# Kernel optimization log

Hardware: AMD Instinct MI355X
Metric: run time of the kernel (lower is better)

Reference implementation:

```python
import jax, jax.numpy as jnp
import numpy as np

IN_FEATURES = 4096
OUT_FEATURES = 4096
TOKENS = 8192
DENSITY = 0.5


def setup_inputs() -> dict:
    key = jax.random.key(0)
    kx, kw, km, kb = jax.random.split(key, 4)
    X = jax.random.normal(kx, (TOKENS, IN_FEATURES), dtype=jnp.float32)
    # kaiming-uniform-like init for weight [out, in]
    bound_w = np.sqrt(6.0 / IN_FEATURES) / np.sqrt(1.0 + 5.0)
    W = jax.random.uniform(kw, (OUT_FEATURES, IN_FEATURES), dtype=jnp.float32,
                           minval=-bound_w, maxval=bound_w)
    mask = jax.random.bernoulli(km, DENSITY, (OUT_FEATURES, IN_FEATURES))
    bound_b = 1.0 / np.sqrt(IN_FEATURES)
    b = jax.random.uniform(kb, (OUT_FEATURES,), dtype=jnp.float32,
                           minval=-bound_b, maxval=bound_b)
    return {"X": X, "W": W, "mask": mask, "b": b}


def reference(X, W, mask, b):
    # F.linear with a fixed-mask sparse weight: y = X @ (W * mask)^T + b
    Wm = W * mask.astype(W.dtype)  # masked weight [out, in]
    return jnp.einsum('ti,oi->to', X, Wm) + b
```

## Files before the change

### kernel.cpp

```cpp
#include <hip/hip_runtime.h>
#include <hip/hip_bf16.h>
#include <cstdint>
#include <cstddef>

#define M_TOK 8192
#define K_IN  4096
#define N_OUT 4096

typedef __attribute__((ext_vector_type(8))) short short8;
typedef __attribute__((ext_vector_type(8))) unsigned short ushort8;
typedef __attribute__((ext_vector_type(4))) float f32x4;

__device__ inline void split_bf16(float x, unsigned short& h, unsigned short& l) {
    unsigned int u = __float_as_uint(x);
    unsigned int hb = (u + 0x7FFFu + ((u >> 16) & 1u)) >> 16;
    h = (unsigned short)hb;
    float hf = __uint_as_float(hb << 16);
    float r = x - hf;
    unsigned int ur = __float_as_uint(r);
    unsigned int lb = (ur + 0x7FFFu + ((ur >> 16) & 1u)) >> 16;
    l = (unsigned short)lb;
}

__global__ void sl_cvt_x(const float* __restrict__ X,
                         unsigned short* __restrict__ hi,
                         unsigned short* __restrict__ lo,
                         int ngroups) {
    int stride = gridDim.x * blockDim.x;
    for (int g = blockIdx.x * blockDim.x + threadIdx.x; g < ngroups; g += stride) {
        const float4* p = (const float4*)X + (size_t)g * 2;
        float4 a = p[0], b = p[1];
        float f[8] = {a.x, a.y, a.z, a.w, b.x, b.y, b.z, b.w};
        ushort8 h, l;
#pragma unroll
        for (int i = 0; i < 8; ++i) {
            unsigned short hh, ll;
            split_bf16(f[i], hh, ll);
            h[i] = hh; l[i] = ll;
        }
        *(ushort8*)(hi + (size_t)g * 8) = h;
        *(ushort8*)(lo + (size_t)g * 8) = l;
    }
}

__global__ void sl_cvt_w(const float* __restrict__ W,
                         const int* __restrict__ mask,
                         unsigned short* __restrict__ hi,
                         unsigned short* __restrict__ lo,
                         int ngroups) {
    int stride = gridDim.x * blockDim.x;
    for (int g = blockIdx.x * blockDim.x + threadIdx.x; g < ngroups; g += stride) {
        const float4* p = (const float4*)W + (size_t)g * 2;
        const int4*  mp = (const int4*)mask + (size_t)g * 2;
        float4 a = p[0], b = p[1];
        int4 ma = mp[0], mb = mp[1];
        float f[8];
        f[0] = ma.x ? a.x : 0.f;  f[1] = ma.y ? a.y : 0.f;
        f[2] = ma.z ? a.z : 0.f;  f[3] = ma.w ? a.w : 0.f;
        f[4] = mb.x ? b.x : 0.f;  f[5] = mb.y ? b.y : 0.f;
        f[6] = mb.z ? b.z : 0.f;  f[7] = mb.w ? b.w : 0.f;
        ushort8 h, l;
#pragma unroll
        for (int i = 0; i < 8; ++i) {
            unsigned short hh, ll;
            split_bf16(f[i], hh, ll);
            h[i] = hh; l[i] = ll;
        }
        *(ushort8*)(hi + (size_t)g * 8) = h;
        *(ushort8*)(lo + (size_t)g * 8) = l;
    }
}

__device__ inline void gload16(const void* g, void* l) {
    __builtin_amdgcn_global_load_lds(
        (const __attribute__((address_space(1))) void*)g,
        (__attribute__((address_space(3))) void*)l, 16, 0, 0);
}

__global__ __launch_bounds__(256, 3)
void sl_gemm_bf16x3(const unsigned short* __restrict__ Xhi,
                    const unsigned short* __restrict__ Xlo,
                    const unsigned short* __restrict__ Whi,
                    const unsigned short* __restrict__ Wlo,
                    const float* __restrict__ bias,
                    float* __restrict__ out) {
    __shared__ __align__(16) unsigned short At[128 * 64];
    __shared__ __align__(16) unsigned short Bt[128 * 64];

    const int bid = blockIdx.x;
    const int swz = (bid & 7) * 256 + (bid >> 3);
    const int bm = swz >> 5;
    const int bn = swz & 31;
    const int brow = bm * 128;
    const int bcol = bn * 128;

    const int tid = threadIdx.x;
    const int w   = tid >> 6;
    const int l   = tid & 63;
    const int wr  = w >> 1, wc = w & 1;

    const int rlo  = l >> 3;
    const int slot = l & 7;
    const int kb   = slot ^ rlo;
    const unsigned short* aBase = (kb < 4) ? Xhi : Xlo;
    const unsigned short* bBase = (kb < 4) ? Whi : Wlo;
    const int kboff = (kb & 3) * 8;

    const unsigned short* aSrc[4];
    const unsigned short* bSrc[4];
#pragma unroll
    for (int i = 0; i < 4; ++i) {
        const int ar = brow + w * 32 + i * 8 + rlo;
        const int br = bcol + w * 32 + i * 8 + rlo;
        aSrc[i] = aBase + (size_t)ar * K_IN + kboff;
        bSrc[i] = bBase + (size_t)br * K_IN + kboff;
    }

    const int lr = l & 15;
    const int kg = l >> 4;

    f32x4 acc[4][4];
#pragma unroll
    for (int i = 0; i < 4; ++i)
#pragma unroll
        for (int j = 0; j < 4; ++j)
            acc[i][j] = (f32x4){0.f, 0.f, 0.f, 0.f};

    for (int kt = 0; kt < K_IN / 32; ++kt) {
        const int koff = kt * 32;
#pragma unroll
        for (int i = 0; i < 4; ++i) {
            gload16(aSrc[i] + koff, (char*)At + (w * 4 + i) * 1024);
            gload16(bSrc[i] + koff, (char*)Bt + (w * 4 + i) * 1024);
        }
        __syncthreads();

        short8 bhi[4], blo[4];
#pragma unroll
        for (int j = 0; j < 4; ++j) {
            const int rowB = wc * 64 + j * 16 + lr;
            const int sw = rowB & 7;
            bhi[j] = *(const short8*)(Bt + rowB * 64 + ((kg ^ sw) << 3));
            blo[j] = *(const short8*)(Bt + rowB * 64 + (((kg + 4) ^ sw) << 3));
        }
#pragma unroll
        for (int i = 0; i < 4; ++i) {
            const int rowA = wr * 64 + i * 16 + lr;
            const int sw = rowA & 7;
            short8 ahi = *(const short8*)(At + rowA * 64 + ((kg ^ sw) << 3));
            short8 alo = *(const short8*)(At + rowA * 64 + (((kg + 4) ^ sw) << 3));
#pragma unroll
            for (int j = 0; j < 4; ++j) {
                acc[i][j] = __builtin_amdgcn_mfma_f32_16x16x32_bf16(ahi, bhi[j], acc[i][j], 0, 0, 0);
                acc[i][j] = __builtin_amdgcn_mfma_f32_16x16x32_bf16(ahi, blo[j], acc[i][j], 0, 0, 0);
                acc[i][j] = __builtin_amdgcn_mfma_f32_16x16x32_bf16(alo, bhi[j], acc[i][j], 0, 0, 0);
            }
        }
        __syncthreads();
    }

    float bv[4];
#pragma unroll
    for (int j = 0; j < 4; ++j)
        bv[j] = bias[bcol + wc * 64 + j * 16 + lr];
#pragma unroll
    for (int i = 0; i < 4; ++i) {
        const int trow = brow + wr * 64 + i * 16 + kg * 4;
#pragma unroll
        for (int j = 0; j < 4; ++j) {
            const int ocol = bcol + wc * 64 + j * 16 + lr;
#pragma unroll
            for (int r = 0; r < 4; ++r)
                out[(size_t)(trow + r) * N_OUT + ocol] = acc[i][j][r] + bv[j];
        }
    }
}

__global__ void sl_naive(const float* __restrict__ X, const float* __restrict__ W,
                         const int* __restrict__ mask, const float* __restrict__ bias,
                         float* __restrict__ out) {
    int o = blockIdx.x * blockDim.x + threadIdx.x;
    int t = blockIdx.y;
    if (o >= N_OUT) return;
    const float* xr = X + (size_t)t * K_IN;
    const float* wr = W + (size_t)o * K_IN;
    const int*   mr = mask + (size_t)o * K_IN;
    float s = 0.f;
    for (int k = 0; k < K_IN; ++k)
        s += xr[k] * (mr[k] ? wr[k] : 0.f);
    out[(size_t)t * N_OUT + o] = s + bias[o];
}

extern "C" void kernel_launch(void* const* d_in, const int* in_sizes, int n_in,
                              void* d_out, int out_size, void* d_ws, size_t ws_size,
                              hipStream_t stream) {
    (void)in_sizes; (void)n_in; (void)out_size;
    const float* X    = (const float*)d_in[0];
    const float* W    = (const float*)d_in[1];
    const int*   mask = (const int*)d_in[2];
    const float* bias = (const float*)d_in[3];
    float* out = (float*)d_out;

    const size_t xplane = (size_t)M_TOK * K_IN;
    const size_t wplane = (size_t)N_OUT * K_IN;
    const size_t need = (2 * xplane + 2 * wplane) * sizeof(unsigned short);

    if (ws_size < need) {
        dim3 g((N_OUT + 255) / 256, M_TOK);
        sl_naive<<<g, 256, 0, stream>>>(X, W, mask, bias, out);
        return;
    }

    unsigned short* Xhi = (unsigned short*)d_ws;
    unsigned short* Xlo = Xhi + xplane;
    unsigned short* Whi = Xlo + xplane;
    unsigned short* Wlo = Whi + wplane;

    sl_cvt_x<<<2048, 256, 0, stream>>>(X, Xhi, Xlo, (int)(xplane / 8));
    sl_cvt_w<<<2048, 256, 0, stream>>>(W, mask, Whi, Wlo, (int)(wplane / 8));
    sl_gemm_bf16x3<<<2048, 256, 0, stream>>>(Xhi, Xlo, Whi, Wlo, bias, out);
}
```

Measured before the change: 1.237 ms.

## Restructure bf16x3 GEMM into 256x256 tiles with a 4-stage async pipeline

Enlarges the GEMM block tile from 128x128 to 256x256 with 512 threads, and restructures the K loop so the three bf16 product passes (hi*hi, hi*lo, lo*hi) run as three sequential K segments of 128 steps each. It adds a 4-deep LDS ring buffer filled by direct global-to-LDS loads, with manual vmcnt waits, a single barrier per step, and MFMA priority hints. The aim is to hide memory latency and raise operand reuse per byte loaded. In exchange it uses more LDS and registers per block, giving lower occupancy and fewer blocks. The conversion kernels switch to 4-element vectors per thread.

Result: faster. 1.139 ms (-8.0%).

```diff
diff --git a/kernel.cpp b/kernel.cpp
--- a/kernel.cpp
+++ b/kernel.cpp
@@ -6,9 +6,10 @@
 #define M_TOK 8192
 #define K_IN  4096
 #define N_OUT 4096
+#define NKS   384
 
 typedef __attribute__((ext_vector_type(8))) short short8;
-typedef __attribute__((ext_vector_type(8))) unsigned short ushort8;
+typedef __attribute__((ext_vector_type(4))) unsigned short ushort4v;
 typedef __attribute__((ext_vector_type(4))) float f32x4;
 
 __device__ inline void split_bf16(float x, unsigned short& h, unsigned short& l) {
@@ -22,52 +23,45 @@
     l = (unsigned short)lb;
 }
 
-__global__ void sl_cvt_x(const float* __restrict__ X,
-                         unsigned short* __restrict__ hi,
-                         unsigned short* __restrict__ lo,
-                         int ngroups) {
+__global__ __launch_bounds__(256) void sl_cvt_x(const float* __restrict__ X,
+                                                unsigned short* __restrict__ hi,
+                                                unsigned short* __restrict__ lo, int n4) {
     int stride = gridDim.x * blockDim.x;
-    for (int g = blockIdx.x * blockDim.x + threadIdx.x; g < ngroups; g += stride) {
-        const float4* p = (const float4*)X + (size_t)g * 2;
-        float4 a = p[0], b = p[1];
-        float f[8] = {a.x, a.y, a.z, a.w, b.x, b.y, b.z, b.w};
-        ushort8 h, l;
-#pragma unroll
-        for (int i = 0; i < 8; ++i) {
+    for (int g = blockIdx.x * blockDim.x + threadIdx.x; g < n4; g += stride) {
+        float4 v = ((const float4*)X)[g];
+        float f[4] = {v.x, v.y, v.z, v.w};
+        ushort4v h, l;
+#pragma unroll
+        for (int i = 0; i < 4; ++i) {
             unsigned short hh, ll;
             split_bf16(f[i], hh, ll);
             h[i] = hh; l[i] = ll;
         }
-        *(ushort8*)(hi + (size_t)g * 8) = h;
-        *(ushort8*)(lo + (size_t)g * 8) = l;
-    }
-}
-
-__global__ void sl_cvt_w(const float* __restrict__ W,
-                         const int* __restrict__ mask,
-                         unsigned short* __restrict__ hi,
-                         unsigned short* __restrict__ lo,
-                         int ngroups) {
+        ((ushort4v*)hi)[g] = h;
+        ((ushort4v*)lo)[g] = l;
+    }
+}
+
+__global__ __launch_bounds__(256) void sl_cvt_w(const float* __restrict__ W,
+                                                const int* __restrict__ mask,
+                                                unsigned short* __restrict__ hi,
+                                                unsigned short* __restrict__ lo, int n4) {
     int stride = gridDim.x * blockDim.x;
-    for (int g = blockIdx.x * blockDim.x + threadIdx.x; g < ngroups; g += stride) {
-        const float4* p = (const float4*)W + (size_t)g * 2;
-        const int4*  mp = (const int4*)mask + (size_t)g * 2;
-        float4 a = p[0], b = p[1];
-        int4 ma = mp[0], mb = mp[1];
-        float f[8];
-        f[0] = ma.x ? a.x : 0.f;  f[1] = ma.y ? a.y : 0.f;
-        f[2] = ma.z ? a.z : 0.f;  f[3] = ma.w ? a.w : 0.f;
-        f[4] = mb.x ? b.x : 0.f;  f[5] = mb.y ? b.y : 0.f;
-        f[6] = mb.z ? b.z : 0.f;  f[7] = mb.w ? b.w : 0.f;
-        ushort8 h, l;
-#pragma unroll
-        for (int i = 0; i < 8; ++i) {
+    for (int g = blockIdx.x * blockDim.x + threadIdx.x; g < n4; g += stride) {
+        float4 v = ((const float4*)W)[g];
+        int4  mm = ((const int4*)mask)[g];
+        float f[4];
+        f[0] = mm.x ? v.x : 0.f;  f[1] = mm.y ? v.y : 0.f;
+        f[2] = mm.z ? v.z : 0.f;  f[3] = mm.w ? v.w : 0.f;
+        ushort4v h, l;
+#pragma unroll
+        for (int i = 0; i < 4; ++i) {
             unsigned short hh, ll;
             split_bf16(f[i], hh, ll);
             h[i] = hh; l[i] = ll;
         }
-        *(ushort8*)(hi + (size_t)g * 8) = h;
-        *(ushort8*)(lo + (size_t)g * 8) = l;
+        ((ushort4v*)hi)[g] = h;
+        ((ushort4v*)lo)[g] = l;
     }
 }
 
@@ -77,101 +71,130 @@
         (__attribute__((address_space(3))) void*)l, 16, 0, 0);
 }
 
-__global__ __launch_bounds__(256, 3)
+__global__ __launch_bounds__(512, 2)
 void sl_gemm_bf16x3(const unsigned short* __restrict__ Xhi,
                     const unsigned short* __restrict__ Xlo,
                     const unsigned short* __restrict__ Whi,
                     const unsigned short* __restrict__ Wlo,
                     const float* __restrict__ bias,
                     float* __restrict__ out) {
-    __shared__ __align__(16) unsigned short At[128 * 64];
-    __shared__ __align__(16) unsigned short Bt[128 * 64];
+    __shared__ __align__(16) unsigned short As[4][256][32];
+    __shared__ __align__(16) unsigned short Bs[4][256][32];
 
     const int bid = blockIdx.x;
-    const int swz = (bid & 7) * 256 + (bid >> 3);
-    const int bm = swz >> 5;
-    const int bn = swz & 31;
-    const int brow = bm * 128;
-    const int bcol = bn * 128;
+    const int swz = (bid & 7) * 64 + (bid >> 3);
+    const int bm = swz >> 4;
+    const int bn = swz & 15;
+    const int brow = bm * 256;
+    const int bcol = bn * 256;
 
     const int tid = threadIdx.x;
     const int w   = tid >> 6;
+    const int wm  = w >> 2, wn = w & 3;
     const int l   = tid & 63;
-    const int wr  = w >> 1, wc = w & 1;
-
-    const int rlo  = l >> 3;
-    const int slot = l & 7;
-    const int kb   = slot ^ rlo;
-    const unsigned short* aBase = (kb < 4) ? Xhi : Xlo;
-    const unsigned short* bBase = (kb < 4) ? Whi : Wlo;
-    const int kboff = (kb & 3) * 8;
-
-    const unsigned short* aSrc[4];
-    const unsigned short* bSrc[4];
-#pragma unroll
-    for (int i = 0; i < 4; ++i) {
-        const int ar = brow + w * 32 + i * 8 + rlo;
-        const int br = bcol + w * 32 + i * 8 + rlo;
-        aSrc[i] = aBase + (size_t)ar * K_IN + kboff;
-        bSrc[i] = bBase + (size_t)br * K_IN + kboff;
-    }
-
-    const int lr = l & 15;
-    const int kg = l >> 4;
-
-    f32x4 acc[4][4];
-#pragma unroll
-    for (int i = 0; i < 4; ++i)
-#pragma unroll
-        for (int j = 0; j < 4; ++j)
-            acc[i][j] = (f32x4){0.f, 0.f, 0.f, 0.f};
-
-    for (int kt = 0; kt < K_IN / 32; ++kt) {
-        const int koff = kt * 32;
-#pragma unroll
-        for (int i = 0; i < 4; ++i) {
-            gload16(aSrc[i] + koff, (char*)At + (w * 4 + i) * 1024);
-            gload16(bSrc[i] + koff, (char*)Bt + (w * 4 + i) * 1024);
-        }
-        __syncthreads();
-
-        short8 bhi[4], blo[4];
-#pragma unroll
-        for (int j = 0; j < 4; ++j) {
-            const int rowB = wc * 64 + j * 16 + lr;
-            const int sw = rowB & 7;
-            bhi[j] = *(const short8*)(Bt + rowB * 64 + ((kg ^ sw) << 3));
-            blo[j] = *(const short8*)(Bt + rowB * 64 + (((kg + 4) ^ sw) << 3));
-        }
-#pragma unroll
-        for (int i = 0; i < 4; ++i) {
-            const int rowA = wr * 64 + i * 16 + lr;
-            const int sw = rowA & 7;
-            short8 ahi = *(const short8*)(At + rowA * 64 + ((kg ^ sw) << 3));
-            short8 alo = *(const short8*)(At + rowA * 64 + (((kg + 4) ^ sw) << 3));
-#pragma unroll
-            for (int j = 0; j < 4; ++j) {
-                acc[i][j] = __builtin_amdgcn_mfma_f32_16x16x32_bf16(ahi, bhi[j], acc[i][j], 0, 0, 0);
-                acc[i][j] = __builtin_amdgcn_mfma_f32_16x16x32_bf16(ahi, blo[j], acc[i][j], 0, 0, 0);
-                acc[i][j] = __builtin_amdgcn_mfma_f32_16x16x32_bf16(alo, bhi[j], acc[i][j], 0, 0, 0);
-            }
-        }
-        __syncthreads();
-    }
+    const int r   = l & 15;
+    const int kg  = l >> 4;
+
+    const int swzCol = (((tid & 3) ^ ((tid >> 3) & 3)) * 8);
+    const size_t aRow0 = (size_t)(brow + (tid >> 2)) * K_IN + swzCol;
+    const size_t aRow1 = aRow0 + (size_t)128 * K_IN;
+    const size_t bRow0 = (size_t)(bcol + (tid >> 2)) * K_IN + swzCol;
+    const size_t bRow1 = bRow0 + (size_t)128 * K_IN;
+
+    char* AsB = (char*)&As[0][0][0];
+    char* BsB = (char*)&Bs[0][0][0];
+    const int woff = w * 1024;
+
+    const unsigned short* AsE = &As[0][0][0];
+    const unsigned short* BsE = &Bs[0][0][0];
+    const int slotOff = (kg ^ ((r >> 1) & 3)) * 8;
+    const int aBaseE = (wm * 128 + r) * 32 + slotOff;
+    const int bBaseE = (wn * 64 + r) * 32 + slotOff;
+
+    f32x4 acc[8][4];
+#pragma unroll
+    for (int m = 0; m < 8; ++m)
+#pragma unroll
+        for (int n = 0; n < 4; ++n)
+            acc[m][n] = (f32x4){0.f, 0.f, 0.f, 0.f};
+
+#define STAGE_A(s_) do {                                                   \
+    const int seg_ = (s_) >> 7;                                            \
+    const unsigned short* pA_ = (seg_ == 1) ? Xlo : Xhi;                   \
+    const size_t k_ = (size_t)((s_) & 127) * 32;                           \
+    char* d_ = AsB + ((s_) & 3) * 16384 + woff;                            \
+    gload16(pA_ + aRow0 + k_, d_);                                         \
+    gload16(pA_ + aRow1 + k_, d_ + 8192);                                  \
+} while (0)
+
+#define STAGE_B(s_) do {                                                   \
+    const int seg_ = (s_) >> 7;                                            \
+    const unsigned short* pB_ = (seg_ == 2) ? Wlo : Whi;                   \
+    const size_t k_ = (size_t)((s_) & 127) * 32;                           \
+    char* d_ = BsB + ((s_) & 3) * 16384 + woff;                            \
+    gload16(pB_ + bRow0 + k_, d_);                                         \
+    gload16(pB_ + bRow1 + k_, d_ + 8192);                                  \
+} while (0)
+
+    STAGE_A(0); STAGE_B(0);
+    STAGE_A(1); STAGE_B(1);
+    STAGE_A(2); STAGE_B(2);
+
+    for (int s = 0; s < NKS; ++s) {
+        asm volatile("s_waitcnt vmcnt(8)" ::: "memory");
+        __builtin_amdgcn_s_barrier();
+        __builtin_amdgcn_sched_barrier(0);
+
+        const int buf = (s & 3) * 8192;
+        const bool st = (s + 3) < NKS;
+        if (st) STAGE_A(s + 3);
+
+        short8 a[4], b[4];
+#pragma unroll
+        for (int n = 0; n < 4; ++n)
+            b[n] = *(const short8*)(BsE + buf + bBaseE + n * 512);
+#pragma unroll
+        for (int m = 0; m < 4; ++m)
+            a[m] = *(const short8*)(AsE + buf + aBaseE + m * 512);
+
+        __builtin_amdgcn_s_setprio(1);
+#pragma unroll
+        for (int m = 0; m < 4; ++m)
+#pragma unroll
+            for (int n = 0; n < 4; ++n)
+                acc[m][n] = __builtin_amdgcn_mfma_f32_16x16x32_bf16(a[m], b[n], acc[m][n], 0, 0, 0);
+        __builtin_amdgcn_s_setprio(0);
+
+        if (st) STAGE_B(s + 3);
+#pragma unroll
+        for (int m = 0; m < 4; ++m)
+            a[m] = *(const short8*)(AsE + buf + aBaseE + (m + 4) * 512);
+
+        __builtin_amdgcn_s_setprio(1);
+#pragma unroll
+        for (int m = 0; m < 4; ++m)
+#pragma unroll
+            for (int n = 0; n < 4; ++n)
+                acc[m + 4][n] = __builtin_amdgcn_mfma_f32_16x16x32_bf16(a[m], b[n], acc[m + 4][n], 0, 0, 0);
+        __builtin_amdgcn_s_setprio(0);
+    }
+#undef STAGE_A
+#undef STAGE_B
 
     float bv[4];
 #pragma unroll
-    for (int j = 0; j < 4; ++j)
-        bv[j] = bias[bcol + wc * 64 + j * 16 + lr];
-#pragma unroll
-    for (int i = 0; i < 4; ++i) {
-        const int trow = brow + wr * 64 + i * 16 + kg * 4;
-#pragma unroll
-        for (int j = 0; j < 4; ++j) {
-            const int ocol = bcol + wc * 64 + j * 16 + lr;
-#pragma unroll
-            for (int r = 0; r < 4; ++r)
-                out[(size_t)(trow + r) * N_OUT + ocol] = acc[i][j][r] + bv[j];
+    for (int n = 0; n < 4; ++n)
+        bv[n] = bias[bcol + wn * 64 + n * 16 + r];
+    const int colBase = bcol + wn * 64 + r;
+#pragma unroll
+    for (int m = 0; m < 8; ++m) {
+        const size_t rowb = (size_t)(brow + wm * 128 + m * 16 + kg * 4);
+#pragma unroll
+        for (int n = 0; n < 4; ++n) {
+            const size_t c = (size_t)(colBase + n * 16);
+#pragma unroll
+            for (int q = 0; q < 4; ++q)
+                out[(rowb + q) * N_OUT + c] = acc[m][n][q] + bv[n];
         }
     }
 }
@@ -216,7 +239,7 @@
     unsigned short* Whi = Xlo + xplane;
     unsigned short* Wlo = Whi + wplane;
 
-    sl_cvt_x<<<2048, 256, 0, stream>>>(X, Xhi, Xlo, (int)(xplane / 8));
-    sl_cvt_w<<<2048, 256, 0, stream>>>(W, mask, Whi, Wlo, (int)(wplane / 8));
-    sl_gemm_bf16x3<<<2048, 256, 0, stream>>>(Xhi, Xlo, Whi, Wlo, bias, out);
-}
+    sl_cvt_x<<<2048, 256, 0, stream>>>(X, Xhi, Xlo, (int)(xplane / 4));
+    sl_cvt_w<<<2048, 256, 0, stream>>>(W, mask, Whi, Wlo, (int)(wplane / 4));
+    sl_gemm_bf16x3<<<512, 512, 0, stream>>>(Xhi, Xlo, Whi, Wlo, bias, out);
+}
```
